# Kernel optimization log

Hardware: AMD Instinct MI355X
Metric: run time of the kernel (lower is better)

Reference implementation:

```python
import jax, jax.numpy as jnp
import numpy as np

N_CELLS, N_GENES = 10000, 4000
CELL_F, GENE_F = 2000, 50
HID, LAT, NCLUST = 256, 64, 20
N_EDGES = 640000
ALPHA = 1.0


def _lin(key, fan_in, fan_out):
    k1, k2 = jax.random.split(key)
    bound = 1.0 / np.sqrt(fan_in)
    w = jax.random.uniform(k1, (fan_in, fan_out), jnp.float32, -bound, bound)
    b = jax.random.uniform(k2, (fan_out,), jnp.float32, -bound, bound)
    return w, b


def setup_inputs() -> dict:
    key = jax.random.key(0)
    ks = jax.random.split(key, 20)
    inp = {
        'cell_x': jax.random.normal(ks[0], (N_CELLS, CELL_F), jnp.float32),
        'gene_x': jax.random.normal(ks[1], (N_GENES, GENE_F), jnp.float32),
        'edge_row': jax.random.randint(ks[2], (N_EDGES,), 0, N_CELLS),
        'edge_col': jax.random.randint(ks[3], (N_EDGES,), 0, N_GENES),
        'edge_val': jax.random.uniform(ks[4], (N_EDGES,), jnp.float32),
    }
    # layer 0: cell_in=CELL_F, gene_in=GENE_F -> HID
    inp['l0_cs_w'], inp['l0_cs_b'] = _lin(ks[5], CELL_F, HID)
    inp['l0_cn_w'], inp['l0_cn_b'] = _lin(ks[6], GENE_F, HID)
    inp['l0_gs_w'], inp['l0_gs_b'] = _lin(ks[7], GENE_F, HID)
    inp['l0_gn_w'], inp['l0_gn_b'] = _lin(ks[8], CELL_F, HID)
    # layer 1: HID -> HID
    inp['l1_cs_w'], inp['l1_cs_b'] = _lin(ks[9], HID, HID)
    inp['l1_cn_w'], inp['l1_cn_b'] = _lin(ks[10], HID, HID)
    inp['l1_gs_w'], inp['l1_gs_b'] = _lin(ks[11], HID, HID)
    inp['l1_gn_w'], inp['l1_gn_b'] = _lin(ks[12], HID, HID)
    # latent heads and decoders
    inp['cl_w'], inp['cl_b'] = _lin(ks[13], HID, LAT)
    inp['gl_w'], inp['gl_b'] = _lin(ks[14], HID, LAT)
    inp['cd_w'], inp['cd_b'] = _lin(ks[15], LAT, N_GENES)
    inp['gd_w'], inp['gd_b'] = _lin(ks[16], LAT, N_CELLS)
    inp['centers'] = jax.random.normal(ks[17], (NCLUST, LAT), jnp.float32)
    return inp


def _bip_conv(cell_x, gene_x, er, ec, ev,
              cs_w, cs_b, cn_w, cn_b, gs_w, gs_b, gn_w, gn_b):
    # sparse adjacency matmul as gather + segment_sum over edge list
    cell_neigh = jax.ops.segment_sum(ev[:, None] * gene_x[ec], er,
                                     num_segments=cell_x.shape[0])
    gene_neigh = jax.ops.segment_sum(ev[:, None] * cell_x[er], ec,
                                     num_segments=gene_x.shape[0])
    cell_out = jax.nn.relu(cell_x @ cs_w + cs_b + cell_neigh @ cn_w + cn_b)
    gene_out = jax.nn.relu(gene_x @ gs_w + gs_b + gene_neigh @ gn_w + gn_b)
    return cell_out, gene_out


def reference(cell_x, gene_x, edge_row, edge_col, edge_val,
              l0_cs_w, l0_cs_b, l0_cn_w, l0_cn_b, l0_gs_w, l0_gs_b, l0_gn_w, l0_gn_b,
              l1_cs_w, l1_cs_b, l1_cn_w, l1_cn_b, l1_gs_w, l1_gs_b, l1_gn_w, l1_gn_b,
              cl_w, cl_b, gl_w, gl_b, cd_w, cd_b, gd_w, gd_b, centers):
    c, g = _bip_conv(cell_x, gene_x, edge_row, edge_col, edge_val,
                     l0_cs_w, l0_cs_b, l0_cn_w, l0_cn_b,
                     l0_gs_w, l0_gs_b, l0_gn_w, l0_gn_b)
    c, g = _bip_conv(c, g, edge_row, edge_col, edge_val,
                     l1_cs_w, l1_cs_b, l1_cn_w, l1_cn_b,
                     l1_gs_w, l1_gs_b, l1_gn_w, l1_gn_b)
    z_cells = c @ cl_w + cl_b
    z_genes = g @ gl_w + gl_b
    cell_recon = z_cells @ cd_w + cd_b
    gene_recon = z_genes @ gd_w + gd_b
    # Student-t cluster assignment (DEC)
    sq_dist = jnp.sum((z_cells[:, None, :] - centers[None, :, :]) ** 2, axis=-1)
    numerator = (1.0 + sq_dist / ALPHA) ** (-(ALPHA + 1.0) / 2.0)
    q = numerator / jnp.sum(numerator, axis=1, keepdims=True)
    return z_cells, z_genes, cell_recon, gene_recon, q
```

## Files before the change

### kernel.cpp

```cpp
#include <hip/hip_runtime.h>

#define N_CELLS 10000
#define N_GENES 4000
#define CELL_F  2000
#define CELL_FP 2048
#define GENE_F  50
#define GENE_FP 64
#define HID     256
#define LAT     64
#define NCLUST  20
#define N_EDGES 640000

typedef __attribute__((ext_vector_type(8))) short    bf16x8;
typedef __attribute__((ext_vector_type(8))) unsigned short u16x8;
typedef __attribute__((ext_vector_type(4))) float    f32x4;

__device__ __forceinline__ unsigned short f2bf(float f) {
    unsigned int u = __float_as_uint(f);
    unsigned int r = (u + 0x7FFFu + ((u >> 16) & 1u)) >> 16;
    return (unsigned short)r;
}
__device__ __forceinline__ float bf2f(unsigned short h) {
    return __uint_as_float(((unsigned int)h) << 16);
}

#define GLOAD_LDS16(gp, lp) __builtin_amdgcn_global_load_lds( \
    (const __attribute__((address_space(1))) void*)(gp), \
    (__attribute__((address_space(3))) void*)(lp), 16, 0, 0)

struct GemmDesc {
    const unsigned short *A, *BT;
    const float *bias;
    float *C;
    unsigned short *Cbf;
    int M, N, K;
    int gx, nwg, blk0;
};
struct GemmArgs2 { GemmDesc d[2]; };

template<bool BIAS, bool WF32, bool WBF, bool TEPI, bool QTAIL>
__global__ __launch_bounds__(256)
void gemm_multi(GemmArgs2 ga, int qstart,
                const float* __restrict__ zq, const float* __restrict__ cent,
                float* __restrict__ qout)
{
    __shared__ __align__(16) unsigned char smem[16640];
    unsigned short* As = (unsigned short*)smem;
    unsigned short* Bs = As + 4096;

    if (QTAIL && (int)blockIdx.x >= qstart) {
        float* cs = (float*)smem;
        int tid = threadIdx.x;
        for (int l = tid; l < NCLUST * LAT; l += 256) cs[l] = cent[l];
        __syncthreads();
        int c = (blockIdx.x - qstart) * 256 + tid;
        if (c >= N_CELLS) return;
        float zr[LAT];
        #pragma unroll
        for (int k = 0; k < LAT; ++k) zr[k] = zq[(size_t)c * LAT + k];
        float num[NCLUST];
        float denom = 0.0f;
        for (int j = 0; j < NCLUST; ++j) {
            float d = 0.0f;
            #pragma unroll
            for (int k = 0; k < LAT; ++k) {
                float t = zr[k] - cs[j * LAT + k];
                d += t * t;
            }
            float n = 1.0f / (1.0f + d);
            num[j] = n;
            denom += n;
        }
        float inv = 1.0f / denom;
        for (int j = 0; j < NCLUST; ++j) qout[(size_t)c * NCLUST + j] = num[j] * inv;
        return;
    }

    int b = blockIdx.x;
    int p = (b >= ga.d[1].blk0) ? 1 : 0;
    const GemmDesc d = ga.d[p];
    int lin = b - d.blk0;
    int q8 = d.nwg >> 3, r8 = d.nwg & 7;
    int xcd = lin & 7, idx = lin >> 3;
    int wgid = (xcd < r8 ? xcd * (q8 + 1) : r8 * (q8 + 1) + (xcd - r8) * q8) + idx;
    int by = wgid / d.gx;
    int bx = wgid - by * d.gx;

    const int tid  = threadIdx.x;
    const int lane = tid & 63;
    const int w    = tid >> 6;
    const int cn   = lane & 15;
    const int rj   = lane >> 4;
    const int row0 = by * 64;
    const int col0 = bx * 64;

    const int slot0 = (w * 2) * 64 + lane;
    const int slot1 = slot0 + 64;
    const int r0s = slot0 >> 3, s0s = slot0 & 7, c0s = s0s ^ (r0s & 7);
    const int r1s = slot1 >> 3, s1s = slot1 & 7, c1s = s1s ^ (r1s & 7);
    const size_t arow0 = (size_t)min(row0 + r0s, d.M - 1) * d.K + c0s * 8;
    const size_t arow1 = (size_t)min(row0 + r1s, d.M - 1) * d.K + c1s * 8;
    const size_t brow0 = (size_t)(col0 + r0s) * d.K + c0s * 8;
    const size_t brow1 = (size_t)(col0 + r1s) * d.K + c1s * 8;
    unsigned short* ldsA = As + (w * 2) * 512;
    unsigned short* ldsB = Bs + (w * 2) * 512;

    f32x4 acc[4] = {};

    const int rA = w * 16 + cn, swA = rA & 7, abase = rA * 64;
    const int aoff0 = abase + ((rj)     ^ swA) * 8;
    const int aoff1 = abase + ((rj + 4) ^ swA) * 8;

    for (int kt = 0; kt < d.K; kt += 64) {
        GLOAD_LDS16(d.A  + arow0 + kt, ldsA);
        GLOAD_LDS16(d.A  + arow1 + kt, ldsA + 512);
        GLOAD_LDS16(d.BT + brow0 + kt, ldsB);
        GLOAD_LDS16(d.BT + brow1 + kt, ldsB + 512);
        __syncthreads();
        bf16x8 a0 = *(const bf16x8*)&As[aoff0];
        bf16x8 a1 = *(const bf16x8*)&As[aoff1];
        #pragma unroll
        for (int f = 0; f < 4; ++f) {
            int rB = f * 16 + cn, swB = rB & 7, bb = rB * 64;
            bf16x8 b0 = *(const bf16x8*)&Bs[bb + ((rj)     ^ swB) * 8];
            bf16x8 b1 = *(const bf16x8*)&Bs[bb + ((rj + 4) ^ swB) * 8];
            acc[f] = __builtin_amdgcn_mfma_f32_16x16x32_bf16(a0, b0, acc[f], 0, 0, 0);
            acc[f] = __builtin_amdgcn_mfma_f32_16x16x32_bf16(a1, b1, acc[f], 0, 0, 0);
        }
        __syncthreads();
    }

    if (TEPI) {
        float* Cs = (float*)smem;
        #pragma unroll
        for (int f = 0; f < 4; ++f)
            #pragma unroll
            for (int j = 0; j < 4; ++j)
                Cs[(w * 16 + rj * 4 + j) * 65 + f * 16 + cn] = acc[f][j];
        __syncthreads();
        #pragma unroll
        for (int i = 0; i < 4; ++i) {
            int slot = tid + i * 256;
            int rr = slot >> 4, c4 = (slot & 15) * 4;
            int gr = row0 + rr, gc = col0 + c4;
            if (gr < d.M && gc < d.N) {
                const float* cp = &Cs[rr * 65 + c4];
                float4 bv = BIAS ? *(const float4*)&d.bias[gc] : float4{0,0,0,0};
                float4 v;
                v.x = cp[0] + bv.x; v.y = cp[1] + bv.y;
                v.z = cp[2] + bv.z; v.w = cp[3] + bv.w;
                *(float4*)&d.C[(size_t)gr * d.N + gc] = v;
            }
        }
    } else {
        #pragma unroll
        for (int f = 0; f < 4; ++f) {
            int col = col0 + f * 16 + cn;
            if (col >= d.N) continue;
            float bv = BIAS ? d.bias[col] : 0.0f;
            #pragma unroll
            for (int j = 0; j < 4; ++j) {
                int r = row0 + w * 16 + rj * 4 + j;
                if (r < d.M) {
                    float val = acc[f][j] + bv;
                    if (WF32) d.C[(size_t)r * d.N + col] = val;
                    if (WBF)  d.Cbf[(size_t)r * d.N + col] = f2bf(val);
                }
            }
        }
    }
}

struct PackDesc {
    const float* W1; const float* W2; unsigned short* BT;
    int Kr, Kp, N1, N2, Np, xb, blk0;
};
struct PackArgs { PackDesc d[8]; };

#define CNT_BLK   2500
#define CVTC_BLK  10000
#define CVTG_BLK  125
#define PACK_BLK0 (CNT_BLK + CVTC_BLK + CVTG_BLK)

__global__ __launch_bounds__(256)
void prep_kernel(const int* __restrict__ er, const int* __restrict__ ec,
                 int* __restrict__ cnt_c, int* __restrict__ cnt_g,
                 const float* __restrict__ cell_x, unsigned short* __restrict__ cellx_bf,
                 const float* __restrict__ gene_x, unsigned short* __restrict__ genex_bf,
                 PackArgs pa)
{
    __shared__ float tile[32][33];
    int b = blockIdx.x;
    int tid = threadIdx.x;
    if (b < CNT_BLK) {
        int e = b * 256 + tid;
        atomicAdd(&cnt_c[er[e]], 1);
        atomicAdd(&cnt_g[ec[e]], 1);
        return;
    }
    if (b < CNT_BLK + CVTC_BLK) {
        int row = b - CNT_BLK;
        int col = tid * 8;
        u16x8 v = {0, 0, 0, 0, 0, 0, 0, 0};
        if (col < CELL_F) {
            const float* src = cell_x + (size_t)row * CELL_F + col;
            float4 f0 = *(const float4*)src;
            float4 f1 = *(const float4*)(src + 4);
            v[0] = f2bf(f0.x); v[1] = f2bf(f0.y); v[2] = f2bf(f0.z); v[3] = f2bf(f0.w);
            v[4] = f2bf(f1.x); v[5] = f2bf(f1.y); v[6] = f2bf(f1.z); v[7] = f2bf(f1.w);
        }
        ((u16x8*)(cellx_bf + (size_t)row * CELL_FP))[tid] = v;
        return;
    }
    if (b < PACK_BLK0) {
        int idx = (b - CNT_BLK - CVTC_BLK) * 256 + tid;
        int row = idx >> 3, c8 = idx & 7;
        int col = c8 * 8;
        u16x8 v = {0, 0, 0, 0, 0, 0, 0, 0};
        #pragma unroll
        for (int j = 0; j < 8; ++j)
            if (col + j < GENE_F) v[j] = f2bf(gene_x[(size_t)row * GENE_F + col + j]);
        ((u16x8*)(genex_bf + (size_t)row * GENE_FP))[c8] = v;
        return;
    }
    int pb = b;
    int p = 0;
    #pragma unroll
    for (int i = 1; i < 8; ++i) if (pb >= pa.d[i].blk0) p = i;
    const PackDesc d = pa.d[p];
    int local = pb - d.blk0;
    int kb = local % d.xb, nb = local / d.xb;
    int k0 = kb * 32, n0 = nb * 32;
    int tx = tid & 31, ty = tid >> 5;
    #pragma unroll
    for (int yy = 0; yy < 4; ++yy) {
        int k = k0 + ty + yy * 8;
        int n = n0 + tx;
        float v = 0.0f;
        if (k < d.Kr) {
            if (n < d.N1) v = d.W1[(size_t)k * d.N1 + n];
            else if (n < d.N1 + d.N2) v = d.W2[(size_t)k * d.N2 + (n - d.N1)];
        }
        tile[ty + yy * 8][tx] = v;
    }
    __syncthreads();
    #pragma unroll
    for (int yy = 0; yy < 4; ++yy) {
        int n = n0 + ty + yy * 8;
        int k = k0 + tx;
        if (n < d.Np)
            d.BT[(size_t)n * d.Kp + k] = f2bf(tile[tx][ty + yy * 8]);
    }
}

__global__ __launch_bounds__(1024)
void scan2_kernel(const int* __restrict__ cnt_c, int* __restrict__ ptr_c, int* __restrict__ cur_c,
                  const int* __restrict__ cnt_g, int* __restrict__ ptr_g, int* __restrict__ cur_g)
{
    const int* cnt = blockIdx.x ? cnt_g : cnt_c;
    int* ptr = blockIdx.x ? ptr_g : ptr_c;
    int* cur = blockIdx.x ? cur_g : cur_c;
    int  n   = blockIdx.x ? N_GENES : N_CELLS;
    __shared__ int part[1024];
    int t = threadIdx.x;
    int chunk = (n + 1023) / 1024;
    int lo = t * chunk, hi = min(lo + chunk, n);
    int s = 0;
    for (int i = lo; i < hi; ++i) s += cnt[i];
    part[t] = s;
    __syncthreads();
    #pragma unroll
    for (int off = 1; off < 1024; off <<= 1) {
        int v = (t >= off) ? part[t - off] : 0;
        __syncthreads();
        part[t] += v;
        __syncthreads();
    }
    if (t == 1023) ptr[n] = part[1023];
    int run = part[t] - s;
    for (int i = lo; i < hi; ++i) { ptr[i] = run; cur[i] = run; run += cnt[i]; }
}

__global__ void scatter_kernel(const int* __restrict__ er, const int* __restrict__ ec,
                               const float* __restrict__ ev,
                               int* cur_c, int* cur_g,
                               int* __restrict__ ci, float* __restrict__ cv,
                               int* __restrict__ gi, float* __restrict__ gv)
{
    int e = blockIdx.x * blockDim.x + threadIdx.x;
    if (e < N_EDGES) {
        int r = er[e], c = ec[e];
        float v = ev[e];
        int pc = atomicAdd(&cur_c[r], 1);
        ci[pc] = c; cv[pc] = v;
        int pg = atomicAdd(&cur_g[c], 1);
        gi[pg] = r; gv[pg] = v;
    }
}

struct AggSide {
    const int *ptr, *nbr; const float *val;
    const unsigned short *src, *pre;
    const float *b1, *b2;
    unsigned short *out;
};
struct AggArgs { AggSide s[2]; };

__global__ __launch_bounds__(256)
void agg2_kernel(AggArgs aa)
{
    __shared__ __align__(16) float red[4][256];
    int b = blockIdx.x;
    int side = (b >= N_CELLS) ? 1 : 0;
    const AggSide S = aa.s[side];
    int r = side ? b - N_CELLS : b;
    int t = threadIdx.x;
    int w = t >> 6;
    int lane = t & 63;
    int s = S.ptr[r], e = S.ptr[r + 1];
    const ushort4* src4 = (const ushort4*)S.src;
    float4 acc = {0.0f, 0.0f, 0.0f, 0.0f};
    int i = s + w;
    for (; i + 4 < e; i += 8) {
        int   j0 = S.nbr[i],   j1 = S.nbr[i + 4];
        float v0 = S.val[i],   v1 = S.val[i + 4];
        ushort4 a = src4[(size_t)j0 * 128 + 64 + lane];
        ushort4 bb = src4[(size_t)j1 * 128 + 64 + lane];
        acc.x += v0 * bf2f(a.x) + v1 * bf2f(bb.x);
        acc.y += v0 * bf2f(a.y) + v1 * bf2f(bb.y);
        acc.z += v0 * bf2f(a.z) + v1 * bf2f(bb.z);
        acc.w += v0 * bf2f(a.w) + v1 * bf2f(bb.w);
    }
    if (i < e) {
        int j0 = S.nbr[i]; float v0 = S.val[i];
        ushort4 a = src4[(size_t)j0 * 128 + 64 + lane];
        acc.x += v0 * bf2f(a.x);
        acc.y += v0 * bf2f(a.y);
        acc.z += v0 * bf2f(a.z);
        acc.w += v0 * bf2f(a.w);
    }
    *(float4*)&red[w][lane * 4] = acc;
    __syncthreads();
    float x = red[0][t] + red[1][t] + red[2][t] + red[3][t]
            + bf2f(S.pre[(size_t)r * 512 + t]) + S.b1[t] + S.b2[t];
    S.out[(size_t)r * 256 + t] = f2bf(fmaxf(x, 0.0f));
}

extern "C" void kernel_launch(void* const* d_in, const int* in_sizes, int n_in,
                              void* d_out, int out_size, void* d_ws, size_t ws_size,
                              hipStream_t stream)
{
    const float* cell_x  = (const float*)d_in[0];
    const float* gene_x  = (const float*)d_in[1];
    const int*   er      = (const int*)d_in[2];
    const int*   ec      = (const int*)d_in[3];
    const float* ev      = (const float*)d_in[4];
    const float* l0_cs_w = (const float*)d_in[5];  const float* l0_cs_b = (const float*)d_in[6];
    const float* l0_cn_w = (const float*)d_in[7];  const float* l0_cn_b = (const float*)d_in[8];
    const float* l0_gs_w = (const float*)d_in[9];  const float* l0_gs_b = (const float*)d_in[10];
    const float* l0_gn_w = (const float*)d_in[11]; const float* l0_gn_b = (const float*)d_in[12];
    const float* l1_cs_w = (const float*)d_in[13]; const float* l1_cs_b = (const float*)d_in[14];
    const float* l1_cn_w = (const float*)d_in[15]; const float* l1_cn_b = (const float*)d_in[16];
    const float* l1_gs_w = (const float*)d_in[17]; const float* l1_gs_b = (const float*)d_in[18];
    const float* l1_gn_w = (const float*)d_in[19]; const float* l1_gn_b = (const float*)d_in[20];
    const float* cl_w = (const float*)d_in[21]; const float* cl_b = (const float*)d_in[22];
    const float* gl_w = (const float*)d_in[23]; const float* gl_b = (const float*)d_in[24];
    const float* cd_w = (const float*)d_in[25]; const float* cd_b = (const float*)d_in[26];
    const float* gd_w = (const float*)d_in[27]; const float* gd_b = (const float*)d_in[28];
    const float* centers = (const float*)d_in[29];

    float* out = (float*)d_out;
    float* z_cells    = out;
    float* z_genes    = out + 640000;
    float* cell_recon = out + 896000;
    float* gene_recon = out + 40896000;
    float* q          = out + 80896000;

    char* wsp = (char*)d_ws;
    auto alloc = [&](size_t bytes) -> void* {
        void* p = (void*)wsp;
        wsp += (bytes + 255) & ~(size_t)255;
        return p;
    };
    unsigned short* pre_c_bf = (unsigned short*)alloc((size_t)N_CELLS * 512 * 2);
    unsigned short* pre_g_bf = (unsigned short*)alloc((size_t)N_GENES * 512 * 2);
    unsigned short* c1_bf    = (unsigned short*)alloc((size_t)N_CELLS * 256 * 2);
    unsigned short* g1_bf    = (unsigned short*)alloc((size_t)N_GENES * 256 * 2);
    unsigned short* c2_bf    = (unsigned short*)alloc((size_t)N_CELLS * 256 * 2);
    unsigned short* g2_bf    = (unsigned short*)alloc((size_t)N_GENES * 256 * 2);
    unsigned short* zc_bf    = (unsigned short*)alloc((size_t)N_CELLS * 64 * 2);
    unsigned short* zg_bf    = (unsigned short*)alloc((size_t)N_GENES * 64 * 2);
    unsigned short* cellx_bf = (unsigned short*)alloc((size_t)N_CELLS * CELL_FP * 2);
    unsigned short* genex_bf = (unsigned short*)alloc((size_t)N_GENES * GENE_FP * 2);
    unsigned short* W0cT = (unsigned short*)alloc((size_t)512 * CELL_FP * 2);
    unsigned short* W0gT = (unsigned short*)alloc((size_t)512 * GENE_FP * 2);
    unsigned short* W1cT = (unsigned short*)alloc((size_t)512 * HID * 2);
    unsigned short* W1gT = (unsigned short*)alloc((size_t)512 * HID * 2);
    unsigned short* WzcT = (unsigned short*)alloc((size_t)64 * HID * 2);
    unsigned short* WzgT = (unsigned short*)alloc((size_t)64 * HID * 2);
    unsigned short* WdcT = (unsigned short*)alloc((size_t)4032 * 64 * 2);
    unsigned short* WdgT = (unsigned short*)alloc((size_t)10048 * 64 * 2);
    int* cnt_c = (int*)alloc((size_t)(N_CELLS + N_GENES) * 4);
    int* cnt_g = cnt_c + N_CELLS;
    int* ptr_c = (int*)alloc((size_t)(N_CELLS + 1) * 4);
    int* ptr_g = (int*)alloc((size_t)(N_GENES + 1) * 4);
    int* cur_c = (int*)alloc((size_t)N_CELLS * 4);
    int* cur_g = (int*)alloc((size_t)N_GENES * 4);
    int*   ci = (int*)alloc((size_t)N_EDGES * 4);
    float* cv = (float*)alloc((size_t)N_EDGES * 4);
    int*   gi = (int*)alloc((size_t)N_EDGES * 4);
    float* gv = (float*)alloc((size_t)N_EDGES * 4);

    hipMemsetAsync(cnt_c, 0, (size_t)(N_CELLS + N_GENES) * 4, stream);

    {
        PackArgs pa;
        auto set = [&](int i, const float* W1, const float* W2, unsigned short* BT,
                       int Kr, int Kp, int N1, int N2, int Np, int blk0) -> int {
            int xb = Kp / 32, yb = Np / 32;
            pa.d[i] = {W1, W2, BT, Kr, Kp, N1, N2, Np, xb, blk0};
            return blk0 + xb * yb;
        };
        int nb = PACK_BLK0;
        nb = set(0, l0_cs_w, l0_gn_w, W0cT, CELL_F, CELL_FP, HID, HID, 512, nb);
        nb = set(1, l0_gs_w, l0_cn_w, W0gT, GENE_F, GENE_FP, HID, HID, 512, nb);
        nb = set(2, l1_cs_w, l1_gn_w, W1cT, HID, HID, HID, HID, 512, nb);
        nb = set(3, l1_gs_w, l1_cn_w, W1gT, HID, HID, HID, HID, 512, nb);
        nb = set(4, cl_w, nullptr, WzcT, HID, HID, LAT, 0, 64, nb);
        nb = set(5, gl_w, nullptr, WzgT, HID, HID, LAT, 0, 64, nb);
        nb = set(6, cd_w, nullptr, WdcT, LAT, LAT, N_GENES, 0, 4032, nb);
        nb = set(7, gd_w, nullptr, WdgT, LAT, LAT, N_CELLS, 0, 10048, nb);
        prep_kernel<<<nb, 256, 0, stream>>>(er, ec, cnt_c, cnt_g,
                                            cell_x, cellx_bf, gene_x, genex_bf, pa);
    }

    scan2_kernel<<<2, 1024, 0, stream>>>(cnt_c, ptr_c, cur_c, cnt_g, ptr_g, cur_g);
    scatter_kernel<<<(N_EDGES + 255) / 256, 256, 0, stream>>>(er, ec, ev, cur_c, cur_g,
                                                              ci, cv, gi, gv);

    auto mkdesc = [](const unsigned short* A, const unsigned short* BT, const float* bias,
                     float* C, unsigned short* Cbf, int M, int N, int K, int blk0) -> GemmDesc {
        int gx = (N + 63) / 64, gy = (M + 63) / 64;
        return {A, BT, bias, C, Cbf, M, N, K, gx, gx * gy, blk0};
    };

    {
        GemmArgs2 ga;
        ga.d[0] = mkdesc(cellx_bf, W0cT, nullptr, nullptr, pre_c_bf, N_CELLS, 512, CELL_FP, 0);
        ga.d[1] = mkdesc(genex_bf, W0gT, nullptr, nullptr, pre_g_bf, N_GENES, 512, GENE_FP,
                         ga.d[0].nwg);
        gemm_multi<false, false, true, false, false><<<ga.d[1].blk0 + ga.d[1].nwg, 256, 0, stream>>>(
            ga, 1 << 30, nullptr, nullptr, nullptr);
    }

    {
        AggArgs aa;
        aa.s[0] = {ptr_c, ci, cv, pre_g_bf, pre_c_bf, l0_cs_b, l0_cn_b, c1_bf};
        aa.s[1] = {ptr_g, gi, gv, pre_c_bf, pre_g_bf, l0_gs_b, l0_gn_b, g1_bf};
        agg2_kernel<<<N_CELLS + N_GENES, 256, 0, stream>>>(aa);
    }

    {
        GemmArgs2 ga;
        ga.d[0] = mkdesc(c1_bf, W1cT, nullptr, nullptr, pre_c_bf, N_CELLS, 512, HID, 0);
        ga.d[1] = mkdesc(g1_bf, W1gT, nullptr, nullptr, pre_g_bf, N_GENES, 512, HID,
                         ga.d[0].nwg);
        gemm_multi<false, false, true, false, false><<<ga.d[1].blk0 + ga.d[1].nwg, 256, 0, stream>>>(
            ga, 1 << 30, nullptr, nullptr, nullptr);
    }

    {
        AggArgs aa;
        aa.s[0] = {ptr_c, ci, cv, pre_g_bf, pre_c_bf, l1_cs_b, l1_cn_b, c2_bf};
        aa.s[1] = {ptr_g, gi, gv, pre_c_bf, pre_g_bf, l1_gs_b, l1_gn_b, g2_bf};
        agg2_kernel<<<N_CELLS + N_GENES, 256, 0, stream>>>(aa);
    }

    {
        GemmArgs2 ga;
        ga.d[0] = mkdesc(c2_bf, WzcT, cl_b, z_cells, zc_bf, N_CELLS, LAT, HID, 0);
        ga.d[1] = mkdesc(g2_bf, WzgT, gl_b, z_genes, zg_bf, N_GENES, LAT, HID, ga.d[0].nwg);
        gemm_multi<true, true, true, false, false><<<ga.d[1].blk0 + ga.d[1].nwg, 256, 0, stream>>>(
            ga, 1 << 30, nullptr, nullptr, nullptr);
    }

    {
        GemmArgs2 ga;
        ga.d[0] = mkdesc(zc_bf, WdcT, cd_b, cell_recon, nullptr, N_CELLS, N_GENES, LAT, 0);
        ga.d[1] = mkdesc(zg_bf, WdgT, gd_b, gene_recon, nullptr, N_GENES, N_CELLS, LAT,
                         ga.d[0].nwg);
        int qstart = ga.d[1].blk0 + ga.d[1].nwg;
        int qblocks = (N_CELLS + 255) / 256;
        gemm_multi<true, true, false, true, true><<<qstart + qblocks, 256, 0, stream>>>(
            ga, qstart, z_cells, centers, q);
    }
}
```

Measured before the change: 513.7 us.

## Use 128-row GEMM tiles, fuse edge scatter into layer-0 GEMM, unroll aggregation

The GEMM kernel now takes a row-tile template parameter. The two 512-wide projection GEMMs use 128-row tiles so each loaded B tile feeds twice as many MFMAs. The separate CSR scatter kernel is removed and its work runs in extra leading blocks of the first GEMM launch, which saves a launch and lets the scatter atomics overlap with matrix work. The aggregation loop is unrolled to keep four neighbour gathers in flight instead of two, at the cost of more registers and LDS in the larger-tile GEMM.

Measured after the change: 495.2 us. 3.6% less time.

```diff
diff --git a/kernel.cpp b/kernel.cpp
--- a/kernel.cpp
+++ b/kernel.cpp
@@ -37,16 +37,33 @@
     int gx, nwg, blk0;
 };
 struct GemmArgs2 { GemmDesc d[2]; };
-
-template<bool BIAS, bool WF32, bool WBF, bool TEPI, bool QTAIL>
+struct ScatArgs {
+    const int *er, *ec; const float *ev;
+    int *cur_c, *cur_g;
+    int *ci; float *cv; int *gi; float *gv;
+};
+
+template<int TM, bool BIAS, bool WF32, bool WBF, bool TEPI, bool QTAIL, bool SCAT>
 __global__ __launch_bounds__(256)
-void gemm_multi(GemmArgs2 ga, int qstart,
+void gemm_multi(GemmArgs2 ga, int gemm0, int qstart,
                 const float* __restrict__ zq, const float* __restrict__ cent,
-                float* __restrict__ qout)
+                float* __restrict__ qout, ScatArgs sa)
 {
-    __shared__ __align__(16) unsigned char smem[16640];
+    constexpr int SMEM = (TM * 128 + 8192) > 16640 ? (TM * 128 + 8192) : 16640;
+    __shared__ __align__(16) unsigned char smem[SMEM];
     unsigned short* As = (unsigned short*)smem;
-    unsigned short* Bs = As + 4096;
+    unsigned short* Bs = As + TM * 64;
+
+    if (SCAT && (int)blockIdx.x < gemm0) {
+        int e = blockIdx.x * 256 + threadIdx.x;
+        int r = sa.er[e], c = sa.ec[e];
+        float v = sa.ev[e];
+        int pc = atomicAdd(&sa.cur_c[r], 1);
+        sa.ci[pc] = c; sa.cv[pc] = v;
+        int pg = atomicAdd(&sa.cur_g[c], 1);
+        sa.gi[pg] = r; sa.gv[pg] = v;
+        return;
+    }
 
     if (QTAIL && (int)blockIdx.x >= qstart) {
         float* cs = (float*)smem;
@@ -91,52 +108,73 @@
     const int w    = tid >> 6;
     const int cn   = lane & 15;
     const int rj   = lane >> 4;
-    const int row0 = by * 64;
+    const int row0 = by * TM;
     const int col0 = bx * 64;
 
-    const int slot0 = (w * 2) * 64 + lane;
-    const int slot1 = slot0 + 64;
-    const int r0s = slot0 >> 3, s0s = slot0 & 7, c0s = s0s ^ (r0s & 7);
-    const int r1s = slot1 >> 3, s1s = slot1 & 7, c1s = s1s ^ (r1s & 7);
-    const size_t arow0 = (size_t)min(row0 + r0s, d.M - 1) * d.K + c0s * 8;
-    const size_t arow1 = (size_t)min(row0 + r1s, d.M - 1) * d.K + c1s * 8;
-    const size_t brow0 = (size_t)(col0 + r0s) * d.K + c0s * 8;
-    const size_t brow1 = (size_t)(col0 + r1s) * d.K + c1s * 8;
-    unsigned short* ldsA = As + (w * 2) * 512;
+    constexpr int AI = TM / 32;
+    constexpr int MF = TM / 64;
+
+    size_t arow[AI];
+    unsigned short* ldsA[AI];
+    #pragma unroll
+    for (int j = 0; j < AI; ++j) {
+        int slot = (w * AI + j) * 64 + lane;
+        int rs = slot >> 3, ss = slot & 7, cs = ss ^ (rs & 7);
+        arow[j] = (size_t)min(row0 + rs, d.M - 1) * d.K + cs * 8;
+        ldsA[j] = As + (w * AI + j) * 512;
+    }
+    const int sb0 = (w * 2) * 64 + lane;
+    const int sb1 = sb0 + 64;
+    const int rb0 = sb0 >> 3, cb0 = (sb0 & 7) ^ (rb0 & 7);
+    const int rb1 = sb1 >> 3, cb1 = (sb1 & 7) ^ (rb1 & 7);
+    const size_t brow0 = (size_t)(col0 + rb0) * d.K + cb0 * 8;
+    const size_t brow1 = (size_t)(col0 + rb1) * d.K + cb1 * 8;
     unsigned short* ldsB = Bs + (w * 2) * 512;
 
-    f32x4 acc[4] = {};
-
-    const int rA = w * 16 + cn, swA = rA & 7, abase = rA * 64;
-    const int aoff0 = abase + ((rj)     ^ swA) * 8;
-    const int aoff1 = abase + ((rj + 4) ^ swA) * 8;
+    int aoff0[MF], aoff1[MF];
+    #pragma unroll
+    for (int mf = 0; mf < MF; ++mf) {
+        int rA = w * (TM / 4) + mf * 16 + cn, swA = rA & 7, abase = rA * 64;
+        aoff0[mf] = abase + ((rj)     ^ swA) * 8;
+        aoff1[mf] = abase + ((rj + 4) ^ swA) * 8;
+    }
+
+    f32x4 acc[MF][4] = {};
 
     for (int kt = 0; kt < d.K; kt += 64) {
-        GLOAD_LDS16(d.A  + arow0 + kt, ldsA);
-        GLOAD_LDS16(d.A  + arow1 + kt, ldsA + 512);
+        #pragma unroll
+        for (int j = 0; j < AI; ++j) GLOAD_LDS16(d.A + arow[j] + kt, ldsA[j]);
         GLOAD_LDS16(d.BT + brow0 + kt, ldsB);
         GLOAD_LDS16(d.BT + brow1 + kt, ldsB + 512);
         __syncthreads();
-        bf16x8 a0 = *(const bf16x8*)&As[aoff0];
-        bf16x8 a1 = *(const bf16x8*)&As[aoff1];
+        bf16x8 a0[MF], a1[MF];
+        #pragma unroll
+        for (int mf = 0; mf < MF; ++mf) {
+            a0[mf] = *(const bf16x8*)&As[aoff0[mf]];
+            a1[mf] = *(const bf16x8*)&As[aoff1[mf]];
+        }
         #pragma unroll
         for (int f = 0; f < 4; ++f) {
             int rB = f * 16 + cn, swB = rB & 7, bb = rB * 64;
             bf16x8 b0 = *(const bf16x8*)&Bs[bb + ((rj)     ^ swB) * 8];
             bf16x8 b1 = *(const bf16x8*)&Bs[bb + ((rj + 4) ^ swB) * 8];
-            acc[f] = __builtin_amdgcn_mfma_f32_16x16x32_bf16(a0, b0, acc[f], 0, 0, 0);
-            acc[f] = __builtin_amdgcn_mfma_f32_16x16x32_bf16(a1, b1, acc[f], 0, 0, 0);
+            #pragma unroll
+            for (int mf = 0; mf < MF; ++mf) {
+                acc[mf][f] = __builtin_amdgcn_mfma_f32_16x16x32_bf16(a0[mf], b0, acc[mf][f], 0, 0, 0);
+                acc[mf][f] = __builtin_amdgcn_mfma_f32_16x16x32_bf16(a1[mf], b1, acc[mf][f], 0, 0, 0);
+            }
         }
         __syncthreads();
     }
 
     if (TEPI) {
         float* Cs = (float*)smem;
+        __syncthreads();
         #pragma unroll
         for (int f = 0; f < 4; ++f)
             #pragma unroll
             for (int j = 0; j < 4; ++j)
-                Cs[(w * 16 + rj * 4 + j) * 65 + f * 16 + cn] = acc[f][j];
+                Cs[(w * 16 + rj * 4 + j) * 65 + f * 16 + cn] = acc[0][f][j];
         __syncthreads();
         #pragma unroll
         for (int i = 0; i < 4; ++i) {
@@ -145,7 +183,7 @@
             int gr = row0 + rr, gc = col0 + c4;
             if (gr < d.M && gc < d.N) {
                 const float* cp = &Cs[rr * 65 + c4];
-                float4 bv = BIAS ? *(const float4*)&d.bias[gc] : float4{0,0,0,0};
+                float4 bv = BIAS ? *(const float4*)&d.bias[gc] : float4{0, 0, 0, 0};
                 float4 v;
                 v.x = cp[0] + bv.x; v.y = cp[1] + bv.y;
                 v.z = cp[2] + bv.z; v.w = cp[3] + bv.w;
@@ -154,17 +192,20 @@
         }
     } else {
         #pragma unroll
-        for (int f = 0; f < 4; ++f) {
-            int col = col0 + f * 16 + cn;
-            if (col >= d.N) continue;
-            float bv = BIAS ? d.bias[col] : 0.0f;
+        for (int mf = 0; mf < MF; ++mf) {
             #pragma unroll
-            for (int j = 0; j < 4; ++j) {
-                int r = row0 + w * 16 + rj * 4 + j;
-                if (r < d.M) {
-                    float val = acc[f][j] + bv;
-                    if (WF32) d.C[(size_t)r * d.N + col] = val;
-                    if (WBF)  d.Cbf[(size_t)r * d.N + col] = f2bf(val);
+            for (int f = 0; f < 4; ++f) {
+                int col = col0 + f * 16 + cn;
+                if (col >= d.N) continue;
+                float bv = BIAS ? d.bias[col] : 0.0f;
+                #pragma unroll
+                for (int j = 0; j < 4; ++j) {
+                    int r = row0 + w * (TM / 4) + mf * 16 + rj * 4 + j;
+                    if (r < d.M) {
+                        float val = acc[mf][f][j] + bv;
+                        if (WF32) d.C[(size_t)r * d.N + col] = val;
+                        if (WBF)  d.Cbf[(size_t)r * d.N + col] = f2bf(val);
+                    }
                 }
             }
         }
@@ -281,23 +322,6 @@
     for (int i = lo; i < hi; ++i) { ptr[i] = run; cur[i] = run; run += cnt[i]; }
 }
 
-__global__ void scatter_kernel(const int* __restrict__ er, const int* __restrict__ ec,
-                               const float* __restrict__ ev,
-                               int* cur_c, int* cur_g,
-                               int* __restrict__ ci, float* __restrict__ cv,
-                               int* __restrict__ gi, float* __restrict__ gv)
-{
-    int e = blockIdx.x * blockDim.x + threadIdx.x;
-    if (e < N_EDGES) {
-        int r = er[e], c = ec[e];
-        float v = ev[e];
-        int pc = atomicAdd(&cur_c[r], 1);
-        ci[pc] = c; cv[pc] = v;
-        int pg = atomicAdd(&cur_g[c], 1);
-        gi[pg] = r; gv[pg] = v;
-    }
-}
-
 struct AggSide {
     const int *ptr, *nbr; const float *val;
     const unsigned short *src, *pre;
@@ -321,17 +345,21 @@
     const ushort4* src4 = (const ushort4*)S.src;
     float4 acc = {0.0f, 0.0f, 0.0f, 0.0f};
     int i = s + w;
-    for (; i + 4 < e; i += 8) {
-        int   j0 = S.nbr[i],   j1 = S.nbr[i + 4];
-        float v0 = S.val[i],   v1 = S.val[i + 4];
-        ushort4 a = src4[(size_t)j0 * 128 + 64 + lane];
-        ushort4 bb = src4[(size_t)j1 * 128 + 64 + lane];
-        acc.x += v0 * bf2f(a.x) + v1 * bf2f(bb.x);
-        acc.y += v0 * bf2f(a.y) + v1 * bf2f(bb.y);
-        acc.z += v0 * bf2f(a.z) + v1 * bf2f(bb.z);
-        acc.w += v0 * bf2f(a.w) + v1 * bf2f(bb.w);
-    }
-    if (i < e) {
+    for (; i + 12 < e; i += 16) {
+        int   j0 = S.nbr[i],     j1 = S.nbr[i + 4];
+        int   j2 = S.nbr[i + 8], j3 = S.nbr[i + 12];
+        float v0 = S.val[i],     v1 = S.val[i + 4];
+        float v2 = S.val[i + 8], v3 = S.val[i + 12];
+        ushort4 a0 = src4[(size_t)j0 * 128 + 64 + lane];
+        ushort4 a1 = src4[(size_t)j1 * 128 + 64 + lane];
+        ushort4 a2 = src4[(size_t)j2 * 128 + 64 + lane];
+        ushort4 a3 = src4[(size_t)j3 * 128 + 64 + lane];
+        acc.x += v0 * bf2f(a0.x) + v1 * bf2f(a1.x) + v2 * bf2f(a2.x) + v3 * bf2f(a3.x);
+        acc.y += v0 * bf2f(a0.y) + v1 * bf2f(a1.y) + v2 * bf2f(a2.y) + v3 * bf2f(a3.y);
+        acc.z += v0 * bf2f(a0.z) + v1 * bf2f(a1.z) + v2 * bf2f(a2.z) + v3 * bf2f(a3.z);
+        acc.w += v0 * bf2f(a0.w) + v1 * bf2f(a1.w) + v2 * bf2f(a2.w) + v3 * bf2f(a3.w);
+    }
+    for (; i < e; i += 4) {
         int j0 = S.nbr[i]; float v0 = S.val[i];
         ushort4 a = src4[(size_t)j0 * 128 + 64 + lane];
         acc.x += v0 * bf2f(a.x);
@@ -435,22 +463,24 @@
     }
 
     scan2_kernel<<<2, 1024, 0, stream>>>(cnt_c, ptr_c, cur_c, cnt_g, ptr_g, cur_g);
-    scatter_kernel<<<(N_EDGES + 255) / 256, 256, 0, stream>>>(er, ec, ev, cur_c, cur_g,
-                                                              ci, cv, gi, gv);
 
     auto mkdesc = [](const unsigned short* A, const unsigned short* BT, const float* bias,
-                     float* C, unsigned short* Cbf, int M, int N, int K, int blk0) -> GemmDesc {
-        int gx = (N + 63) / 64, gy = (M + 63) / 64;
+                     float* C, unsigned short* Cbf, int M, int N, int K, int TMv,
+                     int blk0) -> GemmDesc {
+        int gx = (N + 63) / 64, gy = (M + TMv - 1) / TMv;
         return {A, BT, bias, C, Cbf, M, N, K, gx, gx * gy, blk0};
     };
+    ScatArgs sa0 = {er, ec, ev, cur_c, cur_g, ci, cv, gi, gv};
+    ScatArgs saN = {};
 
     {
         GemmArgs2 ga;
-        ga.d[0] = mkdesc(cellx_bf, W0cT, nullptr, nullptr, pre_c_bf, N_CELLS, 512, CELL_FP, 0);
-        ga.d[1] = mkdesc(genex_bf, W0gT, nullptr, nullptr, pre_g_bf, N_GENES, 512, GENE_FP,
-                         ga.d[0].nwg);
-        gemm_multi<false, false, true, false, false><<<ga.d[1].blk0 + ga.d[1].nwg, 256, 0, stream>>>(
-            ga, 1 << 30, nullptr, nullptr, nullptr);
+        ga.d[0] = mkdesc(cellx_bf, W0cT, nullptr, nullptr, pre_c_bf, N_CELLS, 512, CELL_FP, 128, CNT_BLK);
+        ga.d[1] = mkdesc(genex_bf, W0gT, nullptr, nullptr, pre_g_bf, N_GENES, 512, GENE_FP, 128,
+                         CNT_BLK + ga.d[0].nwg);
+        gemm_multi<128, false, false, true, false, false, true>
+            <<<ga.d[1].blk0 + ga.d[1].nwg, 256, 0, stream>>>(
+            ga, CNT_BLK, 1 << 30, nullptr, nullptr, nullptr, sa0);
     }
 
     {
@@ -462,11 +492,12 @@
 
     {
         GemmArgs2 ga;
-        ga.d[0] = mkdesc(c1_bf, W1cT, nullptr, nullptr, pre_c_bf, N_CELLS, 512, HID, 0);
-        ga.d[1] = mkdesc(g1_bf, W1gT, nullptr, nullptr, pre_g_bf, N_GENES, 512, HID,
+        ga.d[0] = mkdesc(c1_bf, W1cT, nullptr, nullptr, pre_c_bf, N_CELLS, 512, HID, 128, 0);
+        ga.d[1] = mkdesc(g1_bf, W1gT, nullptr, nullptr, pre_g_bf, N_GENES, 512, HID, 128,
                          ga.d[0].nwg);
-        gemm_multi<false, false, true, false, false><<<ga.d[1].blk0 + ga.d[1].nwg, 256, 0, stream>>>(
-            ga, 1 << 30, nullptr, nullptr, nullptr);
+        gemm_multi<128, false, false, true, false, false, false>
+            <<<ga.d[1].blk0 + ga.d[1].nwg, 256, 0, stream>>>(
+            ga, 0, 1 << 30, nullptr, nullptr, nullptr, saN);
     }
 
     {
@@ -478,20 +509,22 @@
 
     {
         GemmArgs2 ga;
-        ga.d[0] = mkdesc(c2_bf, WzcT, cl_b, z_cells, zc_bf, N_CELLS, LAT, HID, 0);
-        ga.d[1] = mkdesc(g2_bf, WzgT, gl_b, z_genes, zg_bf, N_GENES, LAT, HID, ga.d[0].nwg);
-        gemm_multi<true, true, true, false, false><<<ga.d[1].blk0 + ga.d[1].nwg, 256, 0, stream>>>(
-            ga, 1 << 30, nullptr, nullptr, nullptr);
+        ga.d[0] = mkdesc(c2_bf, WzcT, cl_b, z_cells, zc_bf, N_CELLS, LAT, HID, 64, 0);
+        ga.d[1] = mkdesc(g2_bf, WzgT, gl_b, z_genes, zg_bf, N_GENES, LAT, HID, 64, ga.d[0].nwg);
+        gemm_multi<64, true, true, true, false, false, false>
+            <<<ga.d[1].blk0 + ga.d[1].nwg, 256, 0, stream>>>(
+            ga, 0, 1 << 30, nullptr, nullptr, nullptr, saN);
     }
 
     {
         GemmArgs2 ga;
-        ga.d[0] = mkdesc(zc_bf, WdcT, cd_b, cell_recon, nullptr, N_CELLS, N_GENES, LAT, 0);
-        ga.d[1] = mkdesc(zg_bf, WdgT, gd_b, gene_recon, nullptr, N_GENES, N_CELLS, LAT,
+        ga.d[0] = mkdesc(zc_bf, WdcT, cd_b, cell_recon, nullptr, N_CELLS, N_GENES, LAT, 64, 0);
+        ga.d[1] = mkdesc(zg_bf, WdgT, gd_b, gene_recon, nullptr, N_GENES, N_CELLS, LAT, 64,
                          ga.d[0].nwg);
         int qstart = ga.d[1].blk0 + ga.d[1].nwg;
         int qblocks = (N_CELLS + 255) / 256;
-        gemm_multi<true, true, false, true, true><<<qstart + qblocks, 256, 0, stream>>>(
-            ga, qstart, z_cells, centers, q);
-    }
-}
+        gemm_multi<64, true, true, false, true, true, false>
+            <<<qstart + qblocks, 256, 0, stream>>>(
+            ga, 0, qstart, z_cells, centers, q, saN);
+    }
+}
```
